# Optimization experiments

Hardware: AMD Instinct MI355X
Metric: run time of the kernel (lower is better)

The kernel has to match this reference:

```python
import jax, jax.numpy as jnp
import numpy as np

N = 1024  # codeword length (power of 2)
K = 512   # info bits
BATCH = 65536
NB_STAGES = int(np.log2(N))  # 10


def _gen_indices(n):
    """Stage-wise gather indices; index n points at a sentinel zero column."""
    nb_stages = int(np.log2(n))
    ind_gather = np.full((nb_stages, n + 1), n, dtype=np.int32)
    for s in range(nb_stages):
        ind_range = np.arange(n // 2)
        ind_dest = ind_range * 2 - np.mod(ind_range, 2 ** s)
        ind_gather[s, ind_dest] = ind_dest + 2 ** s
    return ind_gather


def setup_inputs() -> dict:
    key = jax.random.key(0)
    # binary information bits, float32 as in the original layer
    u = jax.random.randint(key, (BATCH, K), 0, 2).astype(jnp.float32)
    frozen_pos = np.arange(N - K)
    info_pos = jnp.asarray(np.setdiff1d(np.arange(N), frozen_pos), dtype=jnp.int32)  # [K]
    ind_gather = jnp.asarray(_gen_indices(N))  # [NB_STAGES, N+1]
    return {"u": u, "info_pos": info_pos, "ind_gather": ind_gather}


def reference(u, info_pos, ind_gather) -> jnp.ndarray:
    b = u.shape[0]
    # scatter info bits into codeword positions; frozen positions stay 0
    c = jnp.zeros((b, N), u.dtype).at[:, info_pos].set(u)
    # append sentinel zero column at index N (gather target for pass-through lanes)
    x = jnp.concatenate([c, jnp.zeros((b, 1), u.dtype)], axis=1)  # [b, N+1]
    # log2(N)-stage butterfly: XOR == add mod 2 for binary values
    for s in range(NB_STAGES):
        x = jnp.mod(x + x[:, ind_gather[s]], 2.0)
    return x[:, :N]
```

## Files before the change

kernel.cpp:

```cpp
#include <hip/hip_runtime.h>


#define PN     1024
#define PK     512
#define PBATCH 65536
#define WORDS  32

__global__ __launch_bounds__(256) void polar_encode_kernel(
    const float* __restrict__ u,
    const int*   __restrict__ info_pos,
    float*       __restrict__ out)
{
    __shared__ int inv[PN];
    const int tid = threadIdx.x;
    #pragma unroll
    for (int i = tid; i < PN; i += 256) inv[i] = -1;
    __syncthreads();
    #pragma unroll
    for (int k = tid; k < PK; k += 256) inv[info_pos[k]] = k;
    __syncthreads();

    const int lane = tid & 63;
    const int wave = tid >> 6;
    const int l31  = lane & 31;
    const int half = lane >> 5;
    const long rA  = (long)blockIdx.x * 8 + wave * 2;
    const long row = rA + half;
    const float* urow = u + row * (long)PK;

    unsigned int word = 0;
    #pragma unroll 8
    for (int c = 0; c < WORDS; ++c) {
        const int p  = c * 32 + l31;
        const int iv = inv[p];
        float v = 0.0f;
        if (iv >= 0) v = urow[iv];
        const unsigned long long m = __ballot(v != 0.0f);
        const unsigned int sel = half ? (unsigned int)(m >> 32) : (unsigned int)m;
        if (l31 == c) word = sel;
    }

    word ^= (word >> 1)  & 0x55555555u;
    word ^= (word >> 2)  & 0x33333333u;
    word ^= (word >> 4)  & 0x0F0F0F0Fu;
    word ^= (word >> 8)  & 0x00FF00FFu;
    word ^= (word >> 16) & 0x0000FFFFu;

    #pragma unroll
    for (int off = 1; off <= 16; off <<= 1) {
        const unsigned int partner =
            (unsigned int)__shfl_xor((int)word, off, 64);
        if ((l31 & off) == 0) word ^= partner;
    }

    float4* out4 = (float4*)out;
    const long base = rA * (PN / 4);
    #pragma unroll
    for (int j = 0; j < 8; ++j) {
        const int f   = j * 64 + lane;
        const int r   = f >> 8;
        const int wir = (f & 255) >> 3;
        const int src = wir + (r << 5);
        const unsigned int b   = (unsigned int)__shfl((int)word, src, 64);
        const unsigned int nib = (b >> ((lane & 7) * 4)) & 0xFu;
        float4 v;
        v.x = (nib & 1u) ? 1.0f : 0.0f;
        v.y = (nib & 2u) ? 1.0f : 0.0f;
        v.z = (nib & 4u) ? 1.0f : 0.0f;
        v.w = (nib & 8u) ? 1.0f : 0.0f;
        out4[base + f] = v;
    }
}

extern "C" void kernel_launch(void* const* d_in, const int* in_sizes, int n_in,
                              void* d_out, int out_size, void* d_ws, size_t ws_size,
                              hipStream_t stream) {
    const float* u        = (const float*)d_in[0];
    const int*   info_pos = (const int*)d_in[1];
    float* out = (float*)d_out;

    const int blocks = PBATCH / 8;
    polar_encode_kernel<<<blocks, 256, 0, stream>>>(u, info_pos, out);
}
```

Baseline: 370.1 us.

## Skip word chunks without info bits and process more rows per block

Builds a per-block bitmask of which 32-position chunks hold any information bit, then skips the gather and ballot for all-frozen chunks, which removes half the chunk loop for this frozen set. Each block now handles 32 rows instead of 8, spreading the shared inverse-index table setup and its two barriers over more rows. The cost is fewer blocks in flight and an added shared atomic during setup.

New measurement: 414.3 us. 11.9% more time.

```diff
diff --git a/kernel.cpp b/kernel.cpp
--- a/kernel.cpp
+++ b/kernel.cpp
@@ -5,6 +5,8 @@
 #define PK     512
 #define PBATCH 65536
 #define WORDS  32
+#define ROWS_PER_BLOCK 32
+#define PAIRS_PER_WAVE 4
 
 __global__ __launch_bounds__(256) void polar_encode_kernel(
     const float* __restrict__ u,
@@ -12,63 +14,77 @@
     float*       __restrict__ out)
 {
     __shared__ int inv[PN];
+    __shared__ unsigned int s_mask;
     const int tid = threadIdx.x;
+    if (tid == 0) s_mask = 0u;
     #pragma unroll
     for (int i = tid; i < PN; i += 256) inv[i] = -1;
     __syncthreads();
     #pragma unroll
-    for (int k = tid; k < PK; k += 256) inv[info_pos[k]] = k;
+    for (int k = tid; k < PK; k += 256) {
+        const int p = info_pos[k];
+        inv[p] = k;
+        atomicOr(&s_mask, 1u << (p >> 5));
+    }
     __syncthreads();
+
+    const unsigned int wmask =
+        (unsigned int)__builtin_amdgcn_readfirstlane((int)s_mask);
 
     const int lane = tid & 63;
     const int wave = tid >> 6;
     const int l31  = lane & 31;
     const int half = lane >> 5;
-    const long rA  = (long)blockIdx.x * 8 + wave * 2;
-    const long row = rA + half;
-    const float* urow = u + row * (long)PK;
-
-    unsigned int word = 0;
-    #pragma unroll 8
-    for (int c = 0; c < WORDS; ++c) {
-        const int p  = c * 32 + l31;
-        const int iv = inv[p];
-        float v = 0.0f;
-        if (iv >= 0) v = urow[iv];
-        const unsigned long long m = __ballot(v != 0.0f);
-        const unsigned int sel = half ? (unsigned int)(m >> 32) : (unsigned int)m;
-        if (l31 == c) word = sel;
-    }
-
-    word ^= (word >> 1)  & 0x55555555u;
-    word ^= (word >> 2)  & 0x33333333u;
-    word ^= (word >> 4)  & 0x0F0F0F0Fu;
-    word ^= (word >> 8)  & 0x00FF00FFu;
-    word ^= (word >> 16) & 0x0000FFFFu;
+    float4* out4 = (float4*)out;
 
     #pragma unroll
-    for (int off = 1; off <= 16; off <<= 1) {
-        const unsigned int partner =
-            (unsigned int)__shfl_xor((int)word, off, 64);
-        if ((l31 & off) == 0) word ^= partner;
-    }
+    for (int it = 0; it < PAIRS_PER_WAVE; ++it) {
+        const long rA = (long)blockIdx.x * ROWS_PER_BLOCK + it * 8 + wave * 2;
+        const float* urow = u + (rA + half) * (long)PK;
 
-    float4* out4 = (float4*)out;
-    const long base = rA * (PN / 4);
-    #pragma unroll
-    for (int j = 0; j < 8; ++j) {
-        const int f   = j * 64 + lane;
-        const int r   = f >> 8;
-        const int wir = (f & 255) >> 3;
-        const int src = wir + (r << 5);
-        const unsigned int b   = (unsigned int)__shfl((int)word, src, 64);
-        const unsigned int nib = (b >> ((lane & 7) * 4)) & 0xFu;
-        float4 v;
-        v.x = (nib & 1u) ? 1.0f : 0.0f;
-        v.y = (nib & 2u) ? 1.0f : 0.0f;
-        v.z = (nib & 4u) ? 1.0f : 0.0f;
-        v.w = (nib & 8u) ? 1.0f : 0.0f;
-        out4[base + f] = v;
+        unsigned int word = 0;
+        #pragma unroll
+        for (int c = 0; c < WORDS; ++c) {
+            if (wmask & (1u << c)) {
+                const int iv = inv[c * 32 + l31];
+                float v = 0.0f;
+                if (iv >= 0) v = urow[iv];
+                const unsigned long long m = __ballot(v != 0.0f);
+                const unsigned int sel =
+                    half ? (unsigned int)(m >> 32) : (unsigned int)m;
+                if (l31 == c) word = sel;
+            }
+        }
+
+        word ^= (word >> 1)  & 0x55555555u;
+        word ^= (word >> 2)  & 0x33333333u;
+        word ^= (word >> 4)  & 0x0F0F0F0Fu;
+        word ^= (word >> 8)  & 0x00FF00FFu;
+        word ^= (word >> 16) & 0x0000FFFFu;
+
+        #pragma unroll
+        for (int off = 1; off <= 16; off <<= 1) {
+            const unsigned int partner =
+                (unsigned int)__shfl_xor((int)word, off, 64);
+            if ((l31 & off) == 0) word ^= partner;
+        }
+
+        const long base = rA * (PN / 4);
+        #pragma unroll
+        for (int j = 0; j < 8; ++j) {
+            const int f   = j * 64 + lane;
+            const int r   = f >> 8;
+            const int wir = (f & 255) >> 3;
+            const int src = wir + (r << 5);
+            const unsigned int b   = (unsigned int)__shfl((int)word, src, 64);
+            const unsigned int nib = (b >> ((lane & 7) * 4)) & 0xFu;
+            float4 v;
+            v.x = (nib & 1u) ? 1.0f : 0.0f;
+            v.y = (nib & 2u) ? 1.0f : 0.0f;
+            v.z = (nib & 4u) ? 1.0f : 0.0f;
+            v.w = (nib & 8u) ? 1.0f : 0.0f;
+            out4[base + f] = v;
+        }
     }
 }
 
@@ -79,6 +95,6 @@
     const int*   info_pos = (const int*)d_in[1];
     float* out = (float*)d_out;
 
-    const int blocks = PBATCH / 8;
+    const int blocks = PBATCH / ROWS_PER_BLOCK;
     polar_encode_kernel<<<blocks, 256, 0, stream>>>(u, info_pos, out);
 }
```
